# Kernel optimization log

Hardware: AMD Instinct MI355X
Metric: run time of the kernel (lower is better)

Reference implementation:

```python
import jax, jax.numpy as jnp
import numpy as np

DIM = 512
HEADS = 8
EPS = 1e-12  # matches torch F.normalize default eps


def setup_inputs() -> dict:
    key = jax.random.key(0)
    k1, k2, k3, k4 = jax.random.split(key, 4)
    x = jax.random.normal(k1, (4, 2048, DIM), dtype=jnp.float32)
    # nn.Linear(dim, dim*3, bias=False): weight [3*dim, dim], y = x @ W.T
    w_qkv = jax.random.normal(k2, (3 * DIM, DIM), dtype=jnp.float32) * (1.0 / np.sqrt(DIM))
    w_out = jax.random.normal(k3, (DIM, DIM), dtype=jnp.float32) * (1.0 / np.sqrt(DIM))
    temperature = jnp.ones((HEADS, 1, 1), dtype=jnp.float32)
    return {"x": x, "w_qkv": w_qkv, "w_out": w_out, "temperature": temperature}


def _l2norm(t):
    # torch F.normalize(dim=-1): t / max(||t||, eps)
    n = jnp.sqrt(jnp.sum(t * t, axis=-1, keepdims=True))
    return t / jnp.maximum(n, EPS)


def reference(x, w_qkv, w_out, temperature):
    b, n, c = x.shape
    h = HEADS
    d = c // h
    qkv = x @ w_qkv.T  # [b, n, 3c]
    qkv = qkv.reshape(b, n, 3, h, d).transpose(2, 0, 3, 1, 4)  # [3, b, h, n, d]
    q, k, v = qkv[0], qkv[1], qkv[2]
    q = _l2norm(q)
    k = _l2norm(k)
    # cosine attention with learned per-head temperature
    attn = jnp.einsum("bhnd,bhmd->bhnm", q, k) * temperature  # temp broadcasts [h,1,1]
    attn = jax.nn.softmax(attn, axis=-1)
    out = jnp.einsum("bhnm,bhmd->bhnd", attn, v)  # [b, h, n, d]
    out = out.transpose(0, 2, 1, 3).reshape(b, n, c)
    return out @ w_out.T
```

## Files before the change

### kernel.cpp

```cpp
#include <hip/hip_runtime.h>
#include <hip/hip_bf16.h>

using bf16x8 = __attribute__((ext_vector_type(8))) short;
using f32x4  = __attribute__((ext_vector_type(4))) float;
using f32x16 = __attribute__((ext_vector_type(16))) float;
using u32x4  = __attribute__((ext_vector_type(4))) unsigned;

__device__ __forceinline__ short f2bf(float f) {
  union { float f; unsigned u; } v; v.f = f;
  unsigned r = (v.u + 0x7FFFu + ((v.u >> 16) & 1u)) >> 16;
  return (short)(unsigned short)r;
}

__device__ __forceinline__ unsigned cvtpk(float lo, float hi) {
  unsigned r;
  asm("v_cvt_pk_bf16_f32 %0, %1, %2" : "=v"(r) : "v"(lo), "v"(hi));
  return r;
}

__device__ __forceinline__ void plswap(unsigned &a, unsigned &b) {
  asm("v_permlane32_swap_b32 %0, %1" : "+v"(a), "+v"(b));
}

#define GLLDS(gp, lp) __builtin_amdgcn_global_load_lds(                        \
    (const __attribute__((address_space(1))) void*)(gp),                       \
    (__attribute__((address_space(3))) void*)(lp), 16, 0, 0)

__global__ __launch_bounds__(256)
void cvt_xw(const float* __restrict__ x, const float* __restrict__ wq,
            short* __restrict__ xb, short* __restrict__ wb)
{
  const int blk = blockIdx.x;
  const float* src;
  short* dst;
  int i;
  if (blk < 2048) { src = x;  dst = xb; i = blk * 256 + threadIdx.x; }
  else            { src = wq; dst = wb; i = (blk - 2048) * 256 + threadIdx.x; }
  float4 lo = *(const float4*)(src + (size_t)i * 8);
  float4 hi = *(const float4*)(src + (size_t)i * 8 + 4);
  uint4 r;
  r.x = cvtpk(lo.x, lo.y);
  r.y = cvtpk(lo.z, lo.w);
  r.z = cvtpk(hi.x, hi.y);
  r.w = cvtpk(hi.z, hi.w);
  *(uint4*)(dst + (size_t)i * 8) = r;
}

__global__ __launch_bounds__(256)
void cvt_f32_bf16(const float* __restrict__ in, short* __restrict__ out, int n8)
{
  int i = blockIdx.x * 256 + threadIdx.x;
  if (i >= n8) return;
  float4 lo = *(const float4*)(in + (size_t)i * 8);
  float4 hi = *(const float4*)(in + (size_t)i * 8 + 4);
  uint4 r;
  r.x = cvtpk(lo.x, lo.y);
  r.y = cvtpk(lo.z, lo.w);
  r.z = cvtpk(hi.x, hi.y);
  r.w = cvtpk(hi.z, hi.w);
  *(uint4*)(out + (size_t)i * 8) = r;
}

__global__ __launch_bounds__(256, 3)
void gemm_qkv(const short* __restrict__ A, const short* __restrict__ B,
              short* __restrict__ outQ, short* __restrict__ outK,
              short* __restrict__ outVt, const float* __restrict__ temp)
{
  __shared__ short As[128 * 64];
  __shared__ short Bs[128 * 64];
  const int Kd = 512;
  const int tid  = threadIdx.x;
  const int lane = tid & 63;
  const int w    = tid >> 6;
  const int wr   = w >> 1, wc = w & 1;
  const int fr   = lane & 15, fq = lane >> 4;
  const int g  = blockIdx.x;
  const int xcd = g & 7, gi = g >> 3;
  const int bm = xcd * 8 + gi / 12;
  const int bn = gi % 12;
  const int rowA = bm * 128, rowB = bn * 128;

  const int lrow8   = lane >> 3;
  const int lchunk8 = ((lane & 7) ^ lrow8) * 8;
  const short* gA0 = A + (size_t)(rowA + w * 8 + lrow8) * Kd + lchunk8;
  const short* gB0 = B + (size_t)(rowB + w * 8 + lrow8) * Kd + lchunk8;
  char* lA0 = (char*)As + w * 1024;
  char* lB0 = (char*)Bs + w * 1024;
  const int rx7 = fr & 7;

  f32x4 acc[4][4];
  #pragma unroll
  for (int m = 0; m < 4; ++m)
    #pragma unroll
    for (int n = 0; n < 4; ++n) acc[m][n] = (f32x4){0.f, 0.f, 0.f, 0.f};

  for (int k0 = 0; k0 < Kd; k0 += 64) {
    #pragma unroll
    for (int i = 0; i < 4; ++i) {
      GLLDS(gA0 + k0 + i * 32 * Kd, lA0 + i * 4096);
      GLLDS(gB0 + k0 + i * 32 * Kd, lB0 + i * 4096);
    }
    __syncthreads();
    #pragma unroll
    for (int s = 0; s < 2; ++s) {
      bf16x8 afr[4], bfr[4];
      #pragma unroll
      for (int m = 0; m < 4; ++m)
        afr[m] = *(const bf16x8*)((char*)As + (wr*64 + m*16 + fr) * 128
                                  + (((s*4 + fq) ^ rx7) << 4));
      #pragma unroll
      for (int n = 0; n < 4; ++n)
        bfr[n] = *(const bf16x8*)((char*)Bs + (wc*64 + n*16 + fr) * 128
                                  + (((s*4 + fq) ^ rx7) << 4));
      #pragma unroll
      for (int m = 0; m < 4; ++m)
        #pragma unroll
        for (int n = 0; n < 4; ++n)
          acc[m][n] = __builtin_amdgcn_mfma_f32_16x16x32_bf16(afr[m], bfr[n], acc[m][n], 0, 0, 0);
    }
    __syncthreads();
  }

  const int gc0   = rowB + wc*64;
  const int slice = gc0 >> 6;
  const int t3    = slice >> 3;
  const int h     = slice & 7;
  if (t3 < 2) {
    float scl[4][4];
    const float tval = (t3 == 0) ? temp[h] * 1.44269504088896f : 1.0f;
    #pragma unroll
    for (int m = 0; m < 4; ++m) {
      #pragma unroll
      for (int r = 0; r < 4; ++r) {
        float ss = 0.f;
        #pragma unroll
        for (int n = 0; n < 4; ++n) ss += acc[m][n][r] * acc[m][n][r];
        #pragma unroll
        for (int off = 1; off < 16; off <<= 1) ss += __shfl_xor(ss, off);
        scl[m][r] = tval / fmaxf(sqrtf(ss), 1e-12f);
      }
    }
    short* dst = (t3 == 0) ? outQ : outK;
    #pragma unroll
    for (int m = 0; m < 4; ++m) {
      #pragma unroll
      for (int r = 0; r < 4; ++r) {
        int rg = rowA + wr*64 + m*16 + fq*4 + r;
        int b = rg >> 11, nn = rg & 2047;
        size_t rowoff = ((size_t)(b*8 + h) * 2048 + nn) * 64;
        #pragma unroll
        for (int n = 0; n < 4; ++n)
          dst[rowoff + n*16 + fr] = f2bf(acc[m][n][r] * scl[m][r]);
      }
    }
  } else {
    #pragma unroll
    for (int m = 0; m < 4; ++m) {
      int rg0 = rowA + wr*64 + m*16 + fq*4;
      int b = rg0 >> 11, nn0 = rg0 & 2047;
      size_t dbase = (size_t)(b*8 + h) * 64;
      #pragma unroll
      for (int n = 0; n < 4; ++n) {
        unsigned lo = cvtpk(acc[m][n][0], acc[m][n][1]);
        unsigned hi = cvtpk(acc[m][n][2], acc[m][n][3]);
        *(uint2*)(outVt + (dbase + n*16 + fr) * 2048 + nn0) = make_uint2(lo, hi);
      }
    }
  }
}

__global__ __launch_bounds__(256, 2)
void gemm_out(const short* __restrict__ A, const short* __restrict__ B,
              float* __restrict__ outC)
{
  __shared__ short As[128 * 64];
  __shared__ short Bs[64 * 64];
  const int Kd = 512, N = 512;
  const int tid  = threadIdx.x;
  const int lane = tid & 63;
  const int w    = tid >> 6;
  const int fr   = lane & 15, fq = lane >> 4;
  const int g  = blockIdx.x;
  const int xcd = g & 7, gi = g >> 3;
  const int bm = xcd * 8 + gi / 8;
  const int bn = gi % 8;
  const int rowA = bm * 128, rowB = bn * 64;

  const int lrow8   = lane >> 3;
  const int lchunk8 = ((lane & 7) ^ lrow8) * 8;
  const short* gA0 = A + (size_t)(rowA + w * 8 + lrow8) * Kd + lchunk8;
  const short* gB0 = B + (size_t)(rowB + w * 8 + lrow8) * Kd + lchunk8;
  char* lA0 = (char*)As + w * 1024;
  char* lB0 = (char*)Bs + w * 1024;
  const int rx7 = fr & 7;

  f32x4 acc[2][4];
  #pragma unroll
  for (int m = 0; m < 2; ++m)
    #pragma unroll
    for (int n = 0; n < 4; ++n) acc[m][n] = (f32x4){0.f, 0.f, 0.f, 0.f};

  for (int k0 = 0; k0 < Kd; k0 += 64) {
    #pragma unroll
    for (int i = 0; i < 4; ++i)
      GLLDS(gA0 + k0 + i * 32 * Kd, lA0 + i * 4096);
    #pragma unroll
    for (int j = 0; j < 2; ++j)
      GLLDS(gB0 + k0 + j * 32 * Kd, lB0 + j * 4096);
    __syncthreads();
    #pragma unroll
    for (int s = 0; s < 2; ++s) {
      bf16x8 afr[2], bfr[4];
      #pragma unroll
      for (int m = 0; m < 2; ++m)
        afr[m] = *(const bf16x8*)((char*)As + (w*32 + m*16 + fr) * 128
                                  + (((s*4 + fq) ^ rx7) << 4));
      #pragma unroll
      for (int n = 0; n < 4; ++n)
        bfr[n] = *(const bf16x8*)((char*)Bs + (n*16 + fr) * 128
                                  + (((s*4 + fq) ^ rx7) << 4));
      #pragma unroll
      for (int m = 0; m < 2; ++m)
        #pragma unroll
        for (int n = 0; n < 4; ++n)
          acc[m][n] = __builtin_amdgcn_mfma_f32_16x16x32_bf16(afr[m], bfr[n], acc[m][n], 0, 0, 0);
    }
    __syncthreads();
  }

  #pragma unroll
  for (int m = 0; m < 2; ++m) {
    int r0 = rowA + w*32 + m*16 + fq*4;
    #pragma unroll
    for (int n = 0; n < 4; ++n) {
      int c = rowB + n*16 + fr;
      #pragma unroll
      for (int r = 0; r < 4; ++r)
        outC[(size_t)(r0 + r) * N + c] = acc[m][n][r];
    }
  }
}

__global__ __launch_bounds__(256, 2)
void attn_fwd(const short* __restrict__ Q, const short* __restrict__ Kt,
              const short* __restrict__ Vt, short* __restrict__ AO,
              const float* __restrict__ temp)
{
  __shared__ short Kl[2][128 * 64];
  __shared__ short Vl[2][64 * 128];
  __shared__ float Ls[4][32];
  const int tid  = threadIdx.x;
  const int lane = tid & 63;
  const int w    = tid >> 6;
  const int l31  = lane & 31;
  const int hi   = lane >> 5;
  const int bh = blockIdx.x;
  const int qt = blockIdx.y;
  const int b = bh >> 3, h = bh & 7;
  const size_t base  = (size_t)bh * 2048 * 64;
  const size_t vbase = (size_t)bh * 64 * 2048;
  const int q0 = qt * 128 + w * 32;

  const short* kp = Kt + base;
  const short* vp = Vt + vbase;

  const int srowK = tid >> 3;
  const int scol8 = (tid & 7) * 8;
  const int scolB = (tid & 7) * 16;
  const int sxorK = (srowK & 7) << 4;
  const int vr0   = tid >> 4;
  const int vcB   = (tid & 15) * 16;
  const int vc8   = (tid & 15) * 8;
  const int sxorV = (vr0 & 7) << 4;
  const int kswz  = (l31 & 7) << 4;

  bf16x8 stK[4], stV[4];
  #define LOAD_TILE(T)                                                              \
    do { int kt_ = (T) * 128;                                                       \
      _Pragma("unroll")                                                             \
      for (int i_ = 0; i_ < 4; ++i_)                                                \
        stK[i_] = *(const bf16x8*)(kp + (size_t)(kt_ + i_*32 + srowK) * 64 + scol8);\
      _Pragma("unroll")                                                             \
      for (int i_ = 0; i_ < 4; ++i_)                                                \
        stV[i_] = *(const bf16x8*)(vp + (size_t)(i_*16 + vr0) * 2048 + kt_ + vc8);  \
    } while (0)
  #define WRITE_TILE(P_)                                                            \
    do {                                                                            \
      _Pragma("unroll")                                                             \
      for (int i_ = 0; i_ < 4; ++i_)                                                \
        *(bf16x8*)((char*)Kl[P_] + (i_*32 + srowK) * 128 + (scolB ^ sxorK)) = stK[i_];\
      _Pragma("unroll")                                                             \
      for (int i_ = 0; i_ < 4; ++i_)                                                \
        *(bf16x8*)((char*)Vl[P_] + (i_*16 + vr0) * 256 + (vcB ^ sxorV)) = stV[i_];  \
    } while (0)

  bf16x8 bq[4];
  #pragma unroll
  for (int dj = 0; dj < 4; ++dj)
    bq[dj] = *(const bf16x8*)(Q + base + (size_t)(q0 + l31) * 64 + dj*16 + hi*8);

  const float Mh = fabsf(temp[h]) * 1.44269504088896f;
  f32x16 cinit;
  #pragma unroll
  for (int r = 0; r < 16; ++r) cinit[r] = -Mh;

  f32x16 o[2];
  #pragma unroll
  for (int td = 0; td < 2; ++td)
    #pragma unroll
    for (int r = 0; r < 16; ++r) o[td][r] = 0.f;
  float lp = 0.f;

  LOAD_TILE(0); WRITE_TILE(0);
  LOAD_TILE(1); WRITE_TILE(1);
  LOAD_TILE(2);
  __syncthreads();

  for (int t = 0; t < 16; ++t) {
    const int p = t & 1;
    const char* kl = (const char*)Kl[p];
    const char* vl = (const char*)Vl[p];

    f32x16 s[4];
    #pragma unroll
    for (int tk = 0; tk < 4; ++tk) {
      f32x16 z = cinit;
      #pragma unroll
      for (int dj = 0; dj < 4; ++dj) {
        bf16x8 ak = *(const bf16x8*)(kl + (tk*32 + l31) * 128 + ((dj*32 + hi*16) ^ kswz));
        z = __builtin_amdgcn_mfma_f32_32x32x16_bf16(ak, bq[dj], z, 0, 0, 0);
      }
      s[tk] = z;
    }
    #pragma unroll
    for (int tk = 0; tk < 4; ++tk)
      #pragma unroll
      for (int r = 0; r < 16; ++r) {
        float pv = __builtin_amdgcn_exp2f(s[tk][r]);
        s[tk][r] = pv;
        lp += pv;
      }
    bf16x8 pa[8];
    #pragma unroll
    for (int tk = 0; tk < 4; ++tk)
      #pragma unroll
      for (int j = 0; j < 2; ++j) {
        unsigned w0 = cvtpk(s[tk][8*j+0], s[tk][8*j+1]);
        unsigned w2 = cvtpk(s[tk][8*j+4], s[tk][8*j+5]);
        unsigned w1 = cvtpk(s[tk][8*j+2], s[tk][8*j+3]);
        unsigned w3 = cvtpk(s[tk][8*j+6], s[tk][8*j+7]);
        plswap(w0, w2);
        plswap(w1, w3);
        u32x4 pw = {w0, w1, w2, w3};
        pa[tk*2 + j] = __builtin_bit_cast(bf16x8, pw);
      }
    #pragma unroll
    for (int td = 0; td < 2; ++td) {
      f32x16 acc = o[td];
      #pragma unroll
      for (int kj = 0; kj < 8; ++kj) {
        bf16x8 bv = *(const bf16x8*)(vl + (td*32 + l31) * 256 + ((kj*32 + hi*16) ^ kswz));
        acc = __builtin_amdgcn_mfma_f32_32x32x16_bf16(pa[kj], bv, acc, 0, 0, 0);
      }
      o[td] = acc;
    }

    if (t < 15) {
      __syncthreads();
      if (t < 14) {
        WRITE_TILE(p);
        if (t < 13) LOAD_TILE(t + 3);
      }
    }
  }
  #undef LOAD_TILE
  #undef WRITE_TILE

  lp += __shfl_xor(lp, 32);
  if (hi == 0) Ls[w][l31] = 1.0f / lp;
  #pragma unroll
  for (int td = 0; td < 2; ++td)
    #pragma unroll
    for (int r = 0; r < 16; ++r) {
      int qr = (r & 3) + 8 * (r >> 2) + 4 * hi;
      float li = Ls[w][qr];
      int row = b * 2048 + q0 + qr;
      int col = h * 64 + td * 32 + l31;
      AO[(size_t)row * 512 + col] = f2bf(o[td][r] * li);
    }
}

extern "C" void kernel_launch(void* const* d_in, const int* in_sizes, int n_in,
                              void* d_out, int out_size, void* d_ws, size_t ws_size,
                              hipStream_t stream)
{
  const float* x     = (const float*)d_in[0];
  const float* w_qkv = (const float*)d_in[1];
  const float* w_out = (const float*)d_in[2];
  const float* temp  = (const float*)d_in[3];
  float* out = (float*)d_out;
  short* ws  = (short*)d_ws;

  const size_t NQ = (size_t)4 * 8 * 2048 * 64;
  short* Qb   = ws;
  short* Kb   = ws + NQ;
  short* Vtb  = ws + 2 * NQ;
  short* AO16 = ws + 3 * NQ;
  short* xb   = ws + 4 * NQ;
  short* wb   = AO16;
  short* wob  = xb;

  cvt_xw<<<dim3(2432), 256, 0, stream>>>(x, w_qkv, xb, wb);
  gemm_qkv<<<dim3(768), 256, 0, stream>>>(xb, wb, Qb, Kb, Vtb, temp);
  cvt_f32_bf16<<<dim3(128), 256, 0, stream>>>(w_out, wob, 32768);
  attn_fwd<<<dim3(32, 16), 256, 0, stream>>>(Qb, Kb, Vtb, AO16, temp);
  gemm_out<<<dim3(512), 256, 0, stream>>>(AO16, wob, out);
}
```

Baseline: 82.15 us.

## Stage K/V tiles with direct global-to-LDS loads in attention kernel

Replaces the register-staged K/V prefetch (global load into registers, then an LDS write after a barrier, three tiles deep) with global_load_lds direct-to-LDS transfers into the double buffer, issued one tile ahead at the start of each iteration. The swizzle moves from the LDS write address to the global source column so the existing XOR-swizzled reads stay valid. This frees the staging registers and the explicit LDS store instructions. In exchange the prefetch depth drops from three tiles to one, which leaves less room to hide global latency, and correctness relies on the barrier at the end of each iteration also waiting for the async LDS loads to complete.

```diff
diff --git a/kernel.cpp b/kernel.cpp
--- a/kernel.cpp
+++ b/kernel.cpp
@@ -264,34 +264,24 @@
   const short* kp = Kt + base;
   const short* vp = Vt + vbase;
 
-  const int srowK = tid >> 3;
-  const int scol8 = (tid & 7) * 8;
-  const int scolB = (tid & 7) * 16;
-  const int sxorK = (srowK & 7) << 4;
-  const int vr0   = tid >> 4;
-  const int vcB   = (tid & 15) * 16;
-  const int vc8   = (tid & 15) * 8;
-  const int sxorV = (vr0 & 7) << 4;
-  const int kswz  = (l31 & 7) << 4;
-
-  bf16x8 stK[4], stV[4];
-  #define LOAD_TILE(T)                                                              \
-    do { int kt_ = (T) * 128;                                                       \
-      _Pragma("unroll")                                                             \
-      for (int i_ = 0; i_ < 4; ++i_)                                                \
-        stK[i_] = *(const bf16x8*)(kp + (size_t)(kt_ + i_*32 + srowK) * 64 + scol8);\
-      _Pragma("unroll")                                                             \
-      for (int i_ = 0; i_ < 4; ++i_)                                                \
-        stV[i_] = *(const bf16x8*)(vp + (size_t)(i_*16 + vr0) * 2048 + kt_ + vc8);  \
-    } while (0)
-  #define WRITE_TILE(P_)                                                            \
-    do {                                                                            \
-      _Pragma("unroll")                                                             \
-      for (int i_ = 0; i_ < 4; ++i_)                                                \
-        *(bf16x8*)((char*)Kl[P_] + (i_*32 + srowK) * 128 + (scolB ^ sxorK)) = stK[i_];\
-      _Pragma("unroll")                                                             \
-      for (int i_ = 0; i_ < 4; ++i_)                                                \
-        *(bf16x8*)((char*)Vl[P_] + (i_*16 + vr0) * 256 + (vcB ^ sxorV)) = stV[i_];  \
+  const int krow   = lane >> 3;
+  const int kchunk = ((lane & 7) ^ krow) * 8;
+  const int vrow = lane >> 4;
+  const int kswz = (l31 & 7) << 4;
+
+  #define STAGE(T, BUF)                                                        \
+    do { int kt_ = (T) * 128;                                                  \
+      _Pragma("unroll")                                                        \
+      for (int il = 0; il < 4; ++il)                                           \
+        GLLDS(kp + (size_t)(kt_ + w*32 + il*8 + krow) * 64 + kchunk,           \
+              (char*)Kl[BUF] + (w*32 + il*8) * 128);                           \
+      _Pragma("unroll")                                                        \
+      for (int il = 0; il < 4; ++il) {                                         \
+        int vr_  = w*16 + il*4 + vrow;                                         \
+        int vch_ = ((lane & 15) ^ (vr_ & 7)) * 8;                              \
+        GLLDS(vp + (size_t)vr_ * 2048 + kt_ + vch_,                            \
+              (char*)Vl[BUF] + (w*16 + il*4) * 256);                           \
+      }                                                                        \
     } while (0)
 
   bf16x8 bq[4];
@@ -311,13 +301,12 @@
     for (int r = 0; r < 16; ++r) o[td][r] = 0.f;
   float lp = 0.f;
 
-  LOAD_TILE(0); WRITE_TILE(0);
-  LOAD_TILE(1); WRITE_TILE(1);
-  LOAD_TILE(2);
+  STAGE(0, 0);
   __syncthreads();
 
   for (int t = 0; t < 16; ++t) {
     const int p = t & 1;
+    if (t < 15) STAGE(t + 1, p ^ 1);
     const char* kl = (const char*)Kl[p];
     const char* vl = (const char*)Vl[p];
 
@@ -365,16 +354,9 @@
       o[td] = acc;
     }
 
-    if (t < 15) {
-      __syncthreads();
-      if (t < 14) {
-        WRITE_TILE(p);
-        if (t < 13) LOAD_TILE(t + 3);
-      }
-    }
+    if (t < 15) __syncthreads();
   }
-  #undef LOAD_TILE
-  #undef WRITE_TILE
+  #undef STAGE
 
   lp += __shfl_xor(lp, 32);
   if (hi == 0) Ls[w][l31] = 1.0f / lp;
```

Result: no change. 82.83 us (+0.8%).
